# Optimization experiments

Hardware: AMD Instinct MI355X
Metric: run time of the kernel (lower is better)

The kernel has to match this reference:

```python
import jax, jax.numpy as jnp
from jax import lax
import numpy as np

B, T, H, W = 2, 16, 128, 128
HID = 256
EPS = 1e-5


def _conv(x, w):
    # x: (N,C,H,W), w: (O,I,3,3), stride 1, pad 1 ('SAME')
    return lax.conv_general_dilated(x, w, (1, 1), 'SAME',
                                    dimension_numbers=('NCHW', 'OIHW', 'NCHW'))


def _cnn_block(x, w, b, g, be, m, v):
    # conv -> BatchNorm (eval mode) -> ReLU -> MaxPool2d(2)
    y = _conv(x, w) + b[None, :, None, None]
    scale = (g * lax.rsqrt(v + EPS))[None, :, None, None]
    shift = (be - m * g * lax.rsqrt(v + EPS))[None, :, None, None]
    y = jax.nn.relu(y * scale + shift)
    return lax.reduce_window(y, -jnp.inf, lax.max,
                             (1, 1, 2, 2), (1, 1, 2, 2), 'VALID')


def _convlstm_layer(xs, Wg, bg):
    # xs: (T,B,Cin,h,w); gate conv on concat([x,h]) -> 4*HID channels
    _, nB, _, h, w = xs.shape
    h0 = jnp.zeros((nB, HID, h, w), xs.dtype)

    def step(carry, x_t):
        hprev, cprev = carry
        z = _conv(jnp.concatenate([x_t, hprev], axis=1), Wg) + bg[None, :, None, None]
        ci, cf, co, cg = jnp.split(z, 4, axis=1)
        c = jax.nn.sigmoid(cf) * cprev + jax.nn.sigmoid(ci) * jnp.tanh(cg)
        hn = jax.nn.sigmoid(co) * jnp.tanh(c)
        return (hn, c), hn

    (_, _), hs = lax.scan(step, (h0, h0), xs)
    return hs  # (T,B,HID,h,w)


def setup_inputs() -> dict:
    key = jax.random.key(0)
    ks = jax.random.split(key, 12)

    def rn(k, shape, s=0.05):
        return jax.random.normal(k, shape, jnp.float32) * s

    inp = {'x': jax.random.normal(ks[0], (B, T, 1, H, W), jnp.float32)}
    chans = [(1, 64), (64, 128), (128, 256)]
    for i, (ci, co) in enumerate(chans):
        inp[f'w{i}'] = rn(ks[1 + i], (co, ci, 3, 3))
        inp[f'b{i}'] = jnp.zeros((co,), jnp.float32)
        inp[f'g{i}'] = jnp.ones((co,), jnp.float32)
        inp[f'be{i}'] = jnp.zeros((co,), jnp.float32)
        inp[f'm{i}'] = rn(ks[4 + i], (co,), 0.01)
        inp[f'v{i}'] = jnp.ones((co,), jnp.float32)
    for l in range(2):
        cin = 256 if l == 0 else HID
        inp[f'lw{l}'] = rn(ks[7 + l], (4 * HID, cin + HID, 3, 3))
        inp[f'lb{l}'] = jnp.zeros((4 * HID,), jnp.float32)
    return inp


def reference(x, w0, b0, g0, be0, m0, v0,
              w1, b1, g1, be1, m1, v1,
              w2, b2, g2, be2, m2, v2,
              lw0, lb0, lw1, lb1):
    nB, nT = x.shape[0], x.shape[1]
    y = x.reshape(nB * nT, x.shape[2], x.shape[3], x.shape[4])
    y = _cnn_block(y, w0, b0, g0, be0, m0, v0)   # (BT,64,64,64)
    y = _cnn_block(y, w1, b1, g1, be1, m1, v1)   # (BT,128,32,32)
    y = _cnn_block(y, w2, b2, g2, be2, m2, v2)   # (BT,256,16,16)
    y = y.reshape(nB, nT, y.shape[1], y.shape[2], y.shape[3])
    xs = jnp.transpose(y, (1, 0, 2, 3, 4))       # (T,B,256,16,16)
    hs = _convlstm_layer(xs, lw0, lb0)
    hs = _convlstm_layer(hs, lw1, lb1)
    z_seq = jnp.transpose(hs, (1, 0, 2, 3, 4))   # (B,T,HID,16,16)
    z_last = z_seq[:, -1]
    return (z_seq, z_last)
```

## Files before the change

### kernel.cpp

```cpp
#include <hip/hip_runtime.h>
#include <hip/hip_bf16.h>
#include <cstddef>
#include <cstdint>

#define BN_EPS 1e-5f

typedef __attribute__((ext_vector_type(8))) _Float16 half8;
typedef __attribute__((ext_vector_type(4))) _Float16 half4;
typedef __attribute__((ext_vector_type(4))) float f32x4;

#define GLOBAL_AS __attribute__((address_space(1)))
#define LDS_AS    __attribute__((address_space(3)))

__device__ __forceinline__ void gload_lds16(const void* g, void* l) {
    __builtin_amdgcn_global_load_lds((const GLOBAL_AS uint32_t*)g,
                                     (LDS_AS uint32_t*)l, 16, 0, 0);
}

__device__ __forceinline__ float sigmoidf_(float x) {
    return 1.f / (1.f + __expf(-x));
}
__device__ __forceinline__ float tanhf_(float x) {
    float e = __expf(2.f * x);
    return 1.f - 2.f / (e + 1.f);
}

template <int CI, int OC, int S, int OCB>
__global__ __launch_bounds__(256) void cnn_block1_kernel(
    const float* __restrict__ in, const float* __restrict__ w,
    const float* __restrict__ bias, const float* __restrict__ g,
    const float* __restrict__ be, const float* __restrict__ m,
    const float* __restrict__ v, _Float16* __restrict__ out)
{
    constexpr int PS  = S / 2;
    constexpr int NQ  = (PS * PS) / 256;
    constexpr int NOG = OC / OCB;
    __shared__ float wl[OCB * CI * 9];

    int bid  = blockIdx.x;
    int quad = bid % NQ;
    int t2   = bid / NQ;
    int ocg  = t2 % NOG;
    int img  = t2 / NOG;
    int tid  = threadIdx.x;
    int oc0  = ocg * OCB;

    const float* wsrc = w + (size_t)oc0 * CI * 9;
    for (int i = tid; i < OCB * CI * 9; i += 256) wl[i] = wsrc[i];
    __syncthreads();

    int pp = quad * 256 + tid;
    int pr = pp / PS, pc = pp % PS;
    int r0 = 2 * pr - 1, c0 = 2 * pc - 1;

    int  roff[4], coff[4];
    bool rok[4], cok[4];
#pragma unroll
    for (int i = 0; i < 4; i++) {
        int rr = r0 + i; rok[i] = (rr >= 0 && rr < S); roff[i] = min(max(rr, 0), S - 1) * S;
        int cc = c0 + i; cok[i] = (cc >= 0 && cc < S); coff[i] = min(max(cc, 0), S - 1);
    }

    float acc[OCB][4];
#pragma unroll
    for (int o = 0; o < OCB; o++)
#pragma unroll
        for (int j = 0; j < 4; j++) acc[o][j] = 0.f;

    const float* ip = in + (size_t)img * CI * S * S;
    for (int ci = 0; ci < CI; ++ci) {
        float patch[4][4];
#pragma unroll
        for (int iy = 0; iy < 4; iy++)
#pragma unroll
            for (int ix = 0; ix < 4; ix++) {
                float val = ip[roff[iy] + coff[ix]];
                patch[iy][ix] = (rok[iy] && cok[ix]) ? val : 0.f;
            }
#pragma unroll
        for (int o = 0; o < OCB; o++) {
            const float* wp = wl + ((size_t)o * CI + ci) * 9;
#pragma unroll
            for (int ky = 0; ky < 3; ky++)
#pragma unroll
                for (int kx = 0; kx < 3; kx++) {
                    float ww = wp[ky * 3 + kx];
                    acc[o][0] += ww * patch[ky][kx];
                    acc[o][1] += ww * patch[ky][kx + 1];
                    acc[o][2] += ww * patch[ky + 1][kx];
                    acc[o][3] += ww * patch[ky + 1][kx + 1];
                }
        }
        ip += S * S;
    }

    half8 hv;
#pragma unroll
    for (int o = 0; o < OCB; o++) {
        int oc = oc0 + o;
        float scale = g[oc] * rsqrtf(v[oc] + BN_EPS);
        float shift = be[oc] - m[oc] * scale + bias[oc] * scale;
        float r00 = fmaxf(acc[o][0] * scale + shift, 0.f);
        float r01 = fmaxf(acc[o][1] * scale + shift, 0.f);
        float r10 = fmaxf(acc[o][2] * scale + shift, 0.f);
        float r11 = fmaxf(acc[o][3] * scale + shift, 0.f);
        hv[o] = (_Float16)fmaxf(fmaxf(r00, r01), fmaxf(r10, r11));
    }
    *(half8*)(&out[((size_t)img * (PS * PS) + pp) * OC + oc0]) = hv;
}

template <int OC, int CI>
__global__ __launch_bounds__(256) void wprep_conv_kernel(
    const float* __restrict__ W, _Float16* __restrict__ Wc)
{
    constexpr int K  = CI * 9;
    constexpr int CH = K / 8;
    int idx = blockIdx.x * 256 + threadIdx.x;
    if (idx >= OC * CH) return;
    int oc = idx / CH, chunk = idx % CH;
    int k0   = chunk * 8;
    int kcp  = (k0 >> 3) & 3;
    int kcl  = kcp ^ ((oc >> 1) & 3);
    int klog = (k0 & ~31) | (kcl << 3);
    int tap = klog / CI, ci = klog % CI;
    const float* src = W + ((size_t)oc * CI + ci) * 9 + tap;
    _Float16* dst = Wc + (size_t)oc * K + k0;
#pragma unroll
    for (int j = 0; j < 8; ++j) dst[j] = (_Float16)src[(size_t)j * 9];
}

__global__ __launch_bounds__(256) void wprep_kernel(
    const float* __restrict__ W, _Float16* __restrict__ Wp)
{
    int idx   = blockIdx.x * 256 + threadIdx.x;
    int row   = idx / 576;
    int chunk = idx % 576;
    int k0    = chunk * 8;
    int kcell = k0 >> 5;
    int kcp   = (k0 >> 3) & 3;
    int kcl   = kcp ^ ((row >> 1) & 3);
    int klog  = kcell * 32 + kcl * 8;
    int c = row >> 2, ggate = row & 3;
    int zc = ggate * 256 + c;
    int part = (klog >= 2304) ? 1 : 0;
    int rem  = klog - part * 2304;
    int tap  = rem >> 8;
    int ci   = rem & 255;
    const float* src = W + (size_t)zc * 4608 + (size_t)(part * 256 + ci) * 9 + tap;
    _Float16* dst = Wp + (size_t)row * 4608 + k0;
#pragma unroll
    for (int j = 0; j < 8; ++j) dst[j] = (_Float16)src[(size_t)j * 9];
}

template <int CI, int OC, int SIN>
__global__ __launch_bounds__(256, 2) void conv_mfma_kernel(
    const _Float16* __restrict__ Wc, const _Float16* __restrict__ in,
    const float* __restrict__ bias, const float* __restrict__ g,
    const float* __restrict__ be, const float* __restrict__ m,
    const float* __restrict__ v, const _Float16* __restrict__ zpage,
    _Float16* __restrict__ out)
{
    constexpr int K    = CI * 9;
    constexpr int KS   = K / 32;
    constexpr int NP   = KS / 2;
    constexpr int SPT  = CI / 32;
    constexpr int NPX  = SIN * SIN;
    constexpr int POOL = SIN / 2;
    constexpr int NPP  = NPX / 4;
    constexpr int NT     = (32 * NPX) / 64;
    constexpr int NCHUNK = NT / 8;

    __shared__ _Float16 Al[6][4096];
    __shared__ _Float16 Bl[6][2048];

    const int tid = threadIdx.x;
    const int gx   = blockIdx.x & 7;
    const int rest = blockIdx.x >> 3;
    const int nb   = gx * NCHUNK + (rest % NCHUNK);
    const int bm   = rest / NCHUNK;

    const int n0  = nb * 64;
    const int img = n0 / NPX;
    const int r   = n0 - img * NPX;

    const int srow = tid >> 2;
    const int kc   = tid & 3;
    const int kcs  = kc ^ ((srow >> 1) & 3);
    const int wid  = tid >> 6;

    const _Float16* aptr  = Wc + (size_t)(bm * 128 + srow) * K + kc * 8;
    const _Float16* aptr2 = aptr + (size_t)64 * K;

    const int rn   = r + srow;
    const int ppix = rn >> 2, quad = rn & 3;
    const int y = (ppix / POOL) * 2 + (quad >> 1);
    const int x = (ppix % POOL) * 2 + (quad & 1);
    const _Float16* imgbase = in + (size_t)img * NPX * CI;

    const int lane = tid & 63;
    const int kq   = lane >> 4;
    const int acol = lane & 15;
    int a_off[2], b_off[4];
#pragma unroll
    for (int mf = 0; mf < 2; mf++) {
        int arow = wid * 32 + mf * 16 + acol;
        a_off[mf] = arow * 64 + ((kq ^ ((arow >> 1) & 3)) << 4);
    }
#pragma unroll
    for (int nf = 0; nf < 4; nf++) {
        int brow = nf * 16 + acol;
        b_off[nf] = brow * 64 + ((kq ^ ((brow >> 1) & 3)) << 4);
    }

    f32x4 acc[2][4];
#pragma unroll
    for (int mf = 0; mf < 2; mf++)
#pragma unroll
        for (int nf = 0; nf < 4; nf++) acc[mf][nf] = {0.f, 0.f, 0.f, 0.f};

    auto stage_pair = [&](int sp, int b2) {
        gload_lds16(aptr  + (size_t)sp * 32,       (char*)&Al[b2][0]            + wid * 1024);
        gload_lds16(aptr  + (size_t)(sp + 1) * 32, (char*)&Al[b2 + 1][0]        + wid * 1024);
        gload_lds16(aptr2 + (size_t)sp * 32,       (char*)&Al[b2][0]     + 4096 + wid * 1024);
        gload_lds16(aptr2 + (size_t)(sp + 1) * 32, (char*)&Al[b2 + 1][0] + 4096 + wid * 1024);
        int tap = sp / SPT;
        int ci0 = (sp % SPT) * 32;
        int dy = tap / 3 - 1, dx = tap - (tap / 3) * 3 - 1;
        int yy = y + dy, xx = x + dx;
        bool ok = (yy >= 0) && (yy < SIN) && (xx >= 0) && (xx < SIN);
        const _Float16* base = ok ? (imgbase + (size_t)(yy * SIN + xx) * CI) : zpage;
        const _Float16* p0 = base + ci0 + kcs * 8;
        gload_lds16(p0,      (char*)&Bl[b2][0]     + wid * 1024);
        gload_lds16(p0 + 32, (char*)&Bl[b2 + 1][0] + wid * 1024);
    };

    stage_pair(0, 0);
    stage_pair(2, 2);

    int cb = 0, ib = 4;
    for (int p = 0; p < NP; ++p) {
        __builtin_amdgcn_sched_barrier(0);
        if (p < NP - 1) asm volatile("s_waitcnt vmcnt(6)" ::: "memory");
        else            asm volatile("s_waitcnt vmcnt(0)" ::: "memory");
        __builtin_amdgcn_s_barrier();
        int sp = 2 * p + 4;
        if (sp < KS) stage_pair(sp, ib);

#pragma unroll
        for (int hs = 0; hs < 2; ++hs) {
            const int bb = cb + hs;
            half8 af[2], bf[4];
#pragma unroll
            for (int mf = 0; mf < 2; mf++)
                af[mf] = *(const half8*)((const char*)&Al[bb][0] + a_off[mf]);
#pragma unroll
            for (int nf = 0; nf < 4; nf++)
                bf[nf] = *(const half8*)((const char*)&Bl[bb][0] + b_off[nf]);
#pragma unroll
            for (int mf = 0; mf < 2; mf++)
#pragma unroll
                for (int nf = 0; nf < 4; nf++)
                    acc[mf][nf] = __builtin_amdgcn_mfma_f32_16x16x32_f16(
                        af[mf], bf[nf], acc[mf][nf], 0, 0, 0);
        }

        cb = (cb == 4) ? 0 : cb + 2;
        ib = (ib == 4) ? 0 : ib + 2;
    }

#pragma unroll
    for (int mf = 0; mf < 2; mf++) {
        const int oc0w = bm * 128 + wid * 32 + mf * 16 + kq * 4;
        float sc[4], sh[4];
#pragma unroll
        for (int j = 0; j < 4; j++) {
            int oc = oc0w + j;
            sc[j] = g[oc] * rsqrtf(v[oc] + BN_EPS);
            sh[j] = be[oc] - m[oc] * sc[j] + bias[oc] * sc[j];
        }
#pragma unroll
        for (int nf = 0; nf < 4; nf++) {
            f32x4 a = acc[mf][nf];
            half4 hv;
#pragma unroll
            for (int j = 0; j < 4; j++) {
                float val = fmaxf(a[j] * sc[j] + sh[j], 0.f);
                val = fmaxf(val, __shfl_xor(val, 1));
                val = fmaxf(val, __shfl_xor(val, 2));
                hv[j] = (_Float16)val;
            }
            if ((acol & 3) == 0) {
                int pl = (r + nf * 16 + acol) >> 2;
                *(half4*)(&out[((size_t)img * NPP + pl) * OC + oc0w]) = hv;
            }
        }
    }
}

struct Seg {
    const _Float16* W;
    const float* lbias;
    const _Float16* hsrc; long hs;
    _Float16* zx;  long zxs;
    float* cstate;
    _Float16* hdst; long hds;
    float* outseq; long osb;
    float* outlast;
    int mode;
};

__global__ __launch_bounds__(256, 4) void lstm3_kernel(
    Seg s0, Seg s1, Seg s2, Seg s3, int e0, int e1, int e2,
    const _Float16* __restrict__ zpage)
{
    __shared__ _Float16 Al[6][2048];
    __shared__ _Float16 Bl[6][1024];

    const int b = blockIdx.x;
    Seg S; int i;
    if (b < e0)      { S = s0; i = b; }
    else if (b < e1) { S = s1; i = b - e0; }
    else if (b < e2) { S = s2; i = b - e1; }
    else             { S = s3; i = b - e2; }

    const int tid = threadIdx.x;
    const int bm  = (i & 7) | (((i >> 3) & 1) << 3);
    const int nn  = i >> 4;
    const int img = nn >> 3;
    const int px0 = (nn & 7) * 32;

    const int wid  = tid >> 6;
    const int lane = tid & 63;
    const int lrow = lane >> 2;
    const int kc   = lane & 3;
    const int rowt = wid * 16 + lrow;
    const int kcs  = kc ^ ((rowt >> 1) & 3);

    const _Float16* aptr = S.W + (size_t)(bm * 64 + rowt) * 4608 + kc * 8;

    const int p_pix = px0 + rowt;
    const int py = p_pix >> 4, px = p_pix & 15;

    const _Float16* srcH = S.hsrc + (size_t)img * S.hs;

    const int kq   = lane >> 4;
    const int acol = lane & 15;
    const int arow = wid * 16 + acol;
    const int a_off  = arow * 64 + ((kq ^ ((arow >> 1) & 3)) << 4);
    const int b_off0 = acol * 64 + ((kq ^ ((acol >> 1) & 3)) << 4);
    const int brow1  = 16 + acol;
    const int b_off1 = brow1 * 64 + ((kq ^ ((brow1 >> 1) & 3)) << 4);

    f32x4 acc0 = {0.f, 0.f, 0.f, 0.f};
    f32x4 acc1 = {0.f, 0.f, 0.f, 0.f};

    const int NPAIR = 36;

    auto stage_pair = [&](int sp, int b2) {
        gload_lds16(aptr + (size_t)sp * 32,       (char*)&Al[b2][0]     + wid * 1024);
        gload_lds16(aptr + (size_t)(sp + 1) * 32, (char*)&Al[b2 + 1][0] + wid * 1024);
        if (wid < 2) {
            int tap = sp >> 3;
            int cc  = sp & 7;
            int t3  = tap / 3;
            int dy = t3 - 1, dx = tap - t3 * 3 - 1;
            int yy = py + dy, xx = px + dx;
            bool ok = (yy >= 0) && (yy < 16) && (xx >= 0) && (xx < 16);
            const _Float16* bsrc = ok ? (srcH + (size_t)(yy * 16 + xx) * 256) : zpage;
            const _Float16* p0 = bsrc + cc * 32 + kcs * 8;
            gload_lds16(p0,      (char*)&Bl[b2][0]     + wid * 1024);
            gload_lds16(p0 + 32, (char*)&Bl[b2 + 1][0] + wid * 1024);
        }
    };

    stage_pair(0, 0);
    stage_pair(2, 2);

    int cb = 0;
    int ib = 4;
    for (int p = 0; p < NPAIR; ++p) {
        __builtin_amdgcn_sched_barrier(0);
        if (wid < 2) {
            if (p < NPAIR - 1) asm volatile("s_waitcnt vmcnt(4)" ::: "memory");
            else               asm volatile("s_waitcnt vmcnt(0)" ::: "memory");
        } else {
            if (p < NPAIR - 1) asm volatile("s_waitcnt vmcnt(2)" ::: "memory");
            else               asm volatile("s_waitcnt vmcnt(0)" ::: "memory");
        }
        __builtin_amdgcn_s_barrier();
        int sp = 2 * p + 4;
        if (sp < 72) stage_pair(sp, ib);

        {
            half8 af  = *(const half8*)((const char*)&Al[cb][0] + a_off);
            half8 bf0 = *(const half8*)((const char*)&Bl[cb][0] + b_off0);
            half8 bf1 = *(const half8*)((const char*)&Bl[cb][0] + b_off1);
            acc0 = __builtin_amdgcn_mfma_f32_16x16x32_f16(af, bf0, acc0, 0, 0, 0);
            acc1 = __builtin_amdgcn_mfma_f32_16x16x32_f16(af, bf1, acc1, 0, 0, 0);
        }
        {
            half8 af  = *(const half8*)((const char*)&Al[cb + 1][0] + a_off);
            half8 bf0 = *(const half8*)((const char*)&Bl[cb + 1][0] + b_off0);
            half8 bf1 = *(const half8*)((const char*)&Bl[cb + 1][0] + b_off1);
            acc0 = __builtin_amdgcn_mfma_f32_16x16x32_f16(af, bf0, acc0, 0, 0, 0);
            acc1 = __builtin_amdgcn_mfma_f32_16x16x32_f16(af, bf1, acc1, 0, 0, 0);
        }

        cb = (cb == 4) ? 0 : cb + 2;
        ib = (ib == 4) ? 0 : ib + 2;
    }

    const int c = bm * 16 + wid * 4 + kq;

    if (S.mode == 1) {
#pragma unroll
        for (int cN = 0; cN < 2; ++cN) {
            f32x4 a = cN ? acc1 : acc0;
            int pxg = px0 + cN * 16 + acol;
            half4 hv;
#pragma unroll
            for (int j = 0; j < 4; j++) hv[j] = (_Float16)a[j];
            *(half4*)(&S.zx[(size_t)img * S.zxs + ((size_t)c * 256 + pxg) * 4]) = hv;
        }
        return;
    }

    float bi  = S.lbias[c];
    float bf_ = S.lbias[256 + c];
    float bo  = S.lbias[512 + c];
    float bg  = S.lbias[768 + c];

#pragma unroll
    for (int cN = 0; cN < 2; ++cN) {
        f32x4 a = cN ? acc1 : acc0;
        int pxg = px0 + cN * 16 + acol;
        half4 zv = *(const half4*)(&S.zx[(size_t)img * S.zxs + ((size_t)c * 256 + pxg) * 4]);
        size_t off = (size_t)img * 65536 + (size_t)c * 256 + pxg;
        float zi = a[0] + (float)zv[0] + bi;
        float zf = a[1] + (float)zv[1] + bf_;
        float zo = a[2] + (float)zv[2] + bo;
        float zg = a[3] + (float)zv[3] + bg;
        float cold = S.cstate[off];
        float cn = sigmoidf_(zf) * cold + sigmoidf_(zi) * tanhf_(zg);
        float hn = sigmoidf_(zo) * tanhf_(cn);
        S.cstate[off] = cn;
        S.hdst[(size_t)img * S.hds + (size_t)pxg * 256 + c] = (_Float16)hn;
        if (S.outseq) {
            S.outseq[(size_t)img * S.osb + (size_t)c * 256 + pxg] = hn;
            if (S.outlast)
                S.outlast[(size_t)img * 65536 + (size_t)c * 256 + pxg] = hn;
        }
    }
}

extern "C" void kernel_launch(void* const* d_in, const int* in_sizes, int n_in,
                              void* d_out, int out_size, void* d_ws, size_t ws_size,
                              hipStream_t stream)
{
    const float* x   = (const float*)d_in[0];
    const float* w0  = (const float*)d_in[1];
    const float* b0  = (const float*)d_in[2];
    const float* g0  = (const float*)d_in[3];
    const float* be0 = (const float*)d_in[4];
    const float* m0  = (const float*)d_in[5];
    const float* v0  = (const float*)d_in[6];
    const float* w1  = (const float*)d_in[7];
    const float* b1  = (const float*)d_in[8];
    const float* g1  = (const float*)d_in[9];
    const float* be1 = (const float*)d_in[10];
    const float* m1  = (const float*)d_in[11];
    const float* v1  = (const float*)d_in[12];
    const float* w2  = (const float*)d_in[13];
    const float* b2  = (const float*)d_in[14];
    const float* g2  = (const float*)d_in[15];
    const float* be2 = (const float*)d_in[16];
    const float* m2  = (const float*)d_in[17];
    const float* v2  = (const float*)d_in[18];
    const float* lw0 = (const float*)d_in[19];
    const float* lb0 = (const float*)d_in[20];
    const float* lw1 = (const float*)d_in[21];
    const float* lb1 = (const float*)d_in[22];

    float* out = (float*)d_out;

    char* base = (char*)d_ws;
    _Float16* Wp0  = (_Float16*)(base);
    _Float16* Wp1  = (_Float16*)(base + 9437184);
    _Float16* h0s  = (_Float16*)(base + 18874368);
    _Float16* y2h  = (_Float16*)(base + 25165824);
    _Float16* Wc2  = (_Float16*)(base + 29360128);
    _Float16* Wc3  = (_Float16*)(base + 29507584);
    _Float16* zpg  = (_Float16*)(base + 30097408);
    _Float16* hb1a = (_Float16*)(base + 30228480);
    _Float16* hb1b = (_Float16*)(base + 30490624);
    float*    cst0 = (float*)(base + 30752768);
    float*    cst1 = (float*)(base + 31277056);
    _Float16* zx1a = (_Float16*)(base + 31801344);
    _Float16* zx1b = (_Float16*)(base + 32849920);
    _Float16* zx0  = (_Float16*)(base + 33898496);
    _Float16* y0   = (_Float16*)(base);
    _Float16* y1   = (_Float16*)(base + 16777216);

    hipMemsetAsync(zpg, 0, 131072, stream);

    cnn_block1_kernel<1, 64, 128, 8><<<32 * 8 * 16, 256, 0, stream>>>(
        x, w0, b0, g0, be0, m0, v0, y0);
    wprep_conv_kernel<128, 64><<<36, 256, 0, stream>>>(w1, Wc2);
    conv_mfma_kernel<64, 128, 64><<<2048, 256, 0, stream>>>(
        Wc2, y0, b1, g1, be1, m1, v1, zpg, y1);
    wprep_conv_kernel<256, 128><<<144, 256, 0, stream>>>(w2, Wc3);
    conv_mfma_kernel<128, 256, 32><<<1024, 256, 0, stream>>>(
        Wc3, y1, b2, g2, be2, m2, v2, zpg, y2h);

    wprep_kernel<<<2304, 256, 0, stream>>>(lw0, Wp0);
    wprep_kernel<<<2304, 256, 0, stream>>>(lw1, Wp1);

    hipMemsetAsync(cst0, 0, (size_t)2 * 524288, stream);

    const long IS = 16 * 65536;

    auto makeD = [&](int t) {
        Seg D{};
        D.W = Wp0; D.lbias = lb0;
        D.hsrc = y2h + (size_t)t * 65536; D.hs = IS;
        D.zx = zx0 + (size_t)t * 262144; D.zxs = 16 * 262144;
        D.cstate = nullptr; D.hdst = nullptr; D.hds = 0;
        D.outseq = nullptr; D.osb = 0; D.outlast = nullptr; D.mode = 1;
        return D;
    };

    {
        Seg D0 = makeD(0), D1 = makeD(1);
        lstm3_kernel<<<512, 256, 0, stream>>>(D0, D1, D1, D1, 256, 512, 512, zpg);
    }

    for (int d = 0; d <= 17; ++d) {
        const bool doA = (d <= 15);
        const bool doC = (d >= 1 && d <= 16);
        const bool doB = (d >= 2);
        const bool doD = (d <= 13);

        Seg segs[4]; int ns = 0; int cum = 0; int ends[4];
        if (doA) {
            int t = d;
            Seg A{};
            A.W = Wp0 + 2304; A.lbias = lb0;
            A.hsrc = (t == 0) ? zpg : (h0s + (size_t)(t - 1) * 65536);
            A.hs   = (t == 0) ? 0 : IS;
            A.zx = zx0 + (size_t)t * 262144; A.zxs = 16 * 262144;
            A.cstate = cst0;
            A.hdst = h0s + (size_t)t * 65536; A.hds = IS;
            A.outseq = nullptr; A.osb = 0; A.outlast = nullptr; A.mode = 0;
            segs[ns] = A; cum += 256; ends[ns++] = cum;
        }
        if (doC) {
            int u = d - 1;
            Seg C{};
            C.W = Wp1; C.lbias = lb1;
            C.hsrc = h0s + (size_t)u * 65536; C.hs = IS;
            C.zx = (u & 1) ? zx1b : zx1a; C.zxs = 262144;
            C.cstate = nullptr; C.hdst = nullptr; C.hds = 0;
            C.outseq = nullptr; C.osb = 0; C.outlast = nullptr; C.mode = 1;
            segs[ns] = C; cum += 256; ends[ns++] = cum;
        }
        if (doB) {
            int v = d - 2;
            Seg B{};
            B.W = Wp1 + 2304; B.lbias = lb1;
            B.hsrc = (v == 0) ? zpg : ((v & 1) ? hb1a : hb1b);
            B.hs   = (v == 0) ? 0 : 65536;
            B.zx = (v & 1) ? zx1b : zx1a; B.zxs = 262144;
            B.cstate = cst1;
            B.hdst = (v & 1) ? hb1b : hb1a; B.hds = 65536;
            B.outseq = out + (size_t)v * 65536; B.osb = 1048576;
            B.outlast = (v == 15) ? (out + 2097152) : nullptr; B.mode = 0;
            segs[ns] = B; cum += 256; ends[ns++] = cum;
        }
        if (doD) {
            segs[ns] = makeD(d + 2); cum += 256; ends[ns++] = cum;
        }
        for (int k = ns; k < 4; ++k) segs[k] = segs[0];
        int e0 = ends[0];
        int e1 = (ns > 1) ? ends[1] : cum;
        int e2 = (ns > 2) ? ends[2] : cum;
        lstm3_kernel<<<cum, 256, 0, stream>>>(
            segs[0], segs[1], segs[2], segs[3], e0, e1, e2, zpg);
    }
}
```

Measured before the change: 573.9 us.

## Halve conv M-tile to 64 rows, merge LSTM weight preps and memsets

The MFMA conv kernels now compute a 64-output-channel tile per block instead of 128. This halves the A-operand LDS buffers and the accumulators, raises the occupancy hint to 3 blocks per CU, and doubles the grid size. The two LSTM weight-prep launches are merged into one kernel, and the zero-page and cell-state memsets are folded into a single contiguous memset to cut launch count. The smaller tile reduces register and LDS pressure but lowers reuse of B-operand data per block, so activation traffic rises.

After: 579.2 us. Within noise of the previous version (+0.9%).

```diff
diff --git a/kernel.cpp b/kernel.cpp
--- a/kernel.cpp
+++ b/kernel.cpp
@@ -129,10 +129,14 @@
     for (int j = 0; j < 8; ++j) dst[j] = (_Float16)src[(size_t)j * 9];
 }
 
-__global__ __launch_bounds__(256) void wprep_kernel(
-    const float* __restrict__ W, _Float16* __restrict__ Wp)
+__global__ __launch_bounds__(256) void wprep2_kernel(
+    const float* __restrict__ W0, _Float16* __restrict__ Wp0o,
+    const float* __restrict__ W1, _Float16* __restrict__ Wp1o)
 {
-    int idx   = blockIdx.x * 256 + threadIdx.x;
+    int gidx = blockIdx.x * 256 + threadIdx.x;
+    const float* W = (gidx < 589824) ? W0 : W1;
+    _Float16* Wp   = (gidx < 589824) ? Wp0o : Wp1o;
+    int idx = (gidx < 589824) ? gidx : (gidx - 589824);
     int row   = idx / 576;
     int chunk = idx % 576;
     int k0    = chunk * 8;
@@ -153,7 +157,7 @@
 }
 
 template <int CI, int OC, int SIN>
-__global__ __launch_bounds__(256, 2) void conv_mfma_kernel(
+__global__ __launch_bounds__(256, 3) void conv_mfma_kernel(
     const _Float16* __restrict__ Wc, const _Float16* __restrict__ in,
     const float* __restrict__ bias, const float* __restrict__ g,
     const float* __restrict__ be, const float* __restrict__ m,
@@ -167,10 +171,11 @@
     constexpr int NPX  = SIN * SIN;
     constexpr int POOL = SIN / 2;
     constexpr int NPP  = NPX / 4;
+    constexpr int MB     = OC / 64;
     constexpr int NT     = (32 * NPX) / 64;
     constexpr int NCHUNK = NT / 8;
 
-    __shared__ _Float16 Al[6][4096];
+    __shared__ _Float16 Al[6][2048];
     __shared__ _Float16 Bl[6][2048];
 
     const int tid = threadIdx.x;
@@ -188,8 +193,7 @@
     const int kcs  = kc ^ ((srow >> 1) & 3);
     const int wid  = tid >> 6;
 
-    const _Float16* aptr  = Wc + (size_t)(bm * 128 + srow) * K + kc * 8;
-    const _Float16* aptr2 = aptr + (size_t)64 * K;
+    const _Float16* aptr = Wc + (size_t)(bm * 64 + srow) * K + kc * 8;
 
     const int rn   = r + srow;
     const int ppix = rn >> 2, quad = rn & 3;
@@ -200,29 +204,22 @@
     const int lane = tid & 63;
     const int kq   = lane >> 4;
     const int acol = lane & 15;
-    int a_off[2], b_off[4];
-#pragma unroll
-    for (int mf = 0; mf < 2; mf++) {
-        int arow = wid * 32 + mf * 16 + acol;
-        a_off[mf] = arow * 64 + ((kq ^ ((arow >> 1) & 3)) << 4);
-    }
+    const int arow = wid * 16 + acol;
+    const int a_off = arow * 64 + ((kq ^ ((arow >> 1) & 3)) << 4);
+    int b_off[4];
 #pragma unroll
     for (int nf = 0; nf < 4; nf++) {
         int brow = nf * 16 + acol;
         b_off[nf] = brow * 64 + ((kq ^ ((brow >> 1) & 3)) << 4);
     }
 
-    f32x4 acc[2][4];
-#pragma unroll
-    for (int mf = 0; mf < 2; mf++)
-#pragma unroll
-        for (int nf = 0; nf < 4; nf++) acc[mf][nf] = {0.f, 0.f, 0.f, 0.f};
+    f32x4 acc[4];
+#pragma unroll
+    for (int nf = 0; nf < 4; nf++) acc[nf] = {0.f, 0.f, 0.f, 0.f};
 
     auto stage_pair = [&](int sp, int b2) {
-        gload_lds16(aptr  + (size_t)sp * 32,       (char*)&Al[b2][0]            + wid * 1024);
-        gload_lds16(aptr  + (size_t)(sp + 1) * 32, (char*)&Al[b2 + 1][0]        + wid * 1024);
-        gload_lds16(aptr2 + (size_t)sp * 32,       (char*)&Al[b2][0]     + 4096 + wid * 1024);
-        gload_lds16(aptr2 + (size_t)(sp + 1) * 32, (char*)&Al[b2 + 1][0] + 4096 + wid * 1024);
+        gload_lds16(aptr + (size_t)sp * 32,       (char*)&Al[b2][0]     + wid * 1024);
+        gload_lds16(aptr + (size_t)(sp + 1) * 32, (char*)&Al[b2 + 1][0] + wid * 1024);
         int tap = sp / SPT;
         int ci0 = (sp % SPT) * 32;
         int dy = tap / 3 - 1, dx = tap - (tap / 3) * 3 - 1;
@@ -240,7 +237,7 @@
     int cb = 0, ib = 4;
     for (int p = 0; p < NP; ++p) {
         __builtin_amdgcn_sched_barrier(0);
-        if (p < NP - 1) asm volatile("s_waitcnt vmcnt(6)" ::: "memory");
+        if (p < NP - 1) asm volatile("s_waitcnt vmcnt(4)" ::: "memory");
         else            asm volatile("s_waitcnt vmcnt(0)" ::: "memory");
         __builtin_amdgcn_s_barrier();
         int sp = 2 * p + 4;
@@ -249,50 +246,40 @@
 #pragma unroll
         for (int hs = 0; hs < 2; ++hs) {
             const int bb = cb + hs;
-            half8 af[2], bf[4];
-#pragma unroll
-            for (int mf = 0; mf < 2; mf++)
-                af[mf] = *(const half8*)((const char*)&Al[bb][0] + a_off[mf]);
-#pragma unroll
-            for (int nf = 0; nf < 4; nf++)
-                bf[nf] = *(const half8*)((const char*)&Bl[bb][0] + b_off[nf]);
-#pragma unroll
-            for (int mf = 0; mf < 2; mf++)
-#pragma unroll
-                for (int nf = 0; nf < 4; nf++)
-                    acc[mf][nf] = __builtin_amdgcn_mfma_f32_16x16x32_f16(
-                        af[mf], bf[nf], acc[mf][nf], 0, 0, 0);
+            half8 af = *(const half8*)((const char*)&Al[bb][0] + a_off);
+#pragma unroll
+            for (int nf = 0; nf < 4; nf++) {
+                half8 bf = *(const half8*)((const char*)&Bl[bb][0] + b_off[nf]);
+                acc[nf] = __builtin_amdgcn_mfma_f32_16x16x32_f16(af, bf, acc[nf], 0, 0, 0);
+            }
         }
 
         cb = (cb == 4) ? 0 : cb + 2;
         ib = (ib == 4) ? 0 : ib + 2;
     }
 
-#pragma unroll
-    for (int mf = 0; mf < 2; mf++) {
-        const int oc0w = bm * 128 + wid * 32 + mf * 16 + kq * 4;
-        float sc[4], sh[4];
+    const int oc0w = bm * 64 + wid * 16 + kq * 4;
+    float sc[4], sh[4];
+#pragma unroll
+    for (int j = 0; j < 4; j++) {
+        int oc = oc0w + j;
+        sc[j] = g[oc] * rsqrtf(v[oc] + BN_EPS);
+        sh[j] = be[oc] - m[oc] * sc[j] + bias[oc] * sc[j];
+    }
+#pragma unroll
+    for (int nf = 0; nf < 4; nf++) {
+        f32x4 a = acc[nf];
+        half4 hv;
 #pragma unroll
         for (int j = 0; j < 4; j++) {
-            int oc = oc0w + j;
-            sc[j] = g[oc] * rsqrtf(v[oc] + BN_EPS);
-            sh[j] = be[oc] - m[oc] * sc[j] + bias[oc] * sc[j];
-        }
-#pragma unroll
-        for (int nf = 0; nf < 4; nf++) {
-            f32x4 a = acc[mf][nf];
-            half4 hv;
-#pragma unroll
-            for (int j = 0; j < 4; j++) {
-                float val = fmaxf(a[j] * sc[j] + sh[j], 0.f);
-                val = fmaxf(val, __shfl_xor(val, 1));
-                val = fmaxf(val, __shfl_xor(val, 2));
-                hv[j] = (_Float16)val;
-            }
-            if ((acol & 3) == 0) {
-                int pl = (r + nf * 16 + acol) >> 2;
-                *(half4*)(&out[((size_t)img * NPP + pl) * OC + oc0w]) = hv;
-            }
+            float val = fmaxf(a[j] * sc[j] + sh[j], 0.f);
+            val = fmaxf(val, __shfl_xor(val, 1));
+            val = fmaxf(val, __shfl_xor(val, 2));
+            hv[j] = (_Float16)val;
+        }
+        if ((acol & 3) == 0) {
+            int pl = (r + nf * 16 + acol) >> 2;
+            *(half4*)(&out[((size_t)img * NPP + pl) * OC + oc0w]) = hv;
         }
     }
 }
@@ -501,21 +488,18 @@
     _Float16* y0   = (_Float16*)(base);
     _Float16* y1   = (_Float16*)(base + 16777216);
 
-    hipMemsetAsync(zpg, 0, 131072, stream);
+    hipMemsetAsync(zpg, 0, (size_t)(31801344 - 30097408), stream);
 
     cnn_block1_kernel<1, 64, 128, 8><<<32 * 8 * 16, 256, 0, stream>>>(
         x, w0, b0, g0, be0, m0, v0, y0);
     wprep_conv_kernel<128, 64><<<36, 256, 0, stream>>>(w1, Wc2);
-    conv_mfma_kernel<64, 128, 64><<<2048, 256, 0, stream>>>(
+    conv_mfma_kernel<64, 128, 64><<<4096, 256, 0, stream>>>(
         Wc2, y0, b1, g1, be1, m1, v1, zpg, y1);
     wprep_conv_kernel<256, 128><<<144, 256, 0, stream>>>(w2, Wc3);
-    conv_mfma_kernel<128, 256, 32><<<1024, 256, 0, stream>>>(
+    conv_mfma_kernel<128, 256, 32><<<2048, 256, 0, stream>>>(
         Wc3, y1, b2, g2, be2, m2, v2, zpg, y2h);
 
-    wprep_kernel<<<2304, 256, 0, stream>>>(lw0, Wp0);
-    wprep_kernel<<<2304, 256, 0, stream>>>(lw1, Wp1);
-
-    hipMemsetAsync(cst0, 0, (size_t)2 * 524288, stream);
+    wprep2_kernel<<<4608, 256, 0, stream>>>(lw0, Wp0, lw1, Wp1);
 
     const long IS = 16 * 65536;
 
```
